# Kernel tuning notes

Hardware: AMD Instinct MI355X
Metric: run time of the kernel (lower is better)

## Reference

```python
import jax, jax.numpy as jnp
import numpy as np

B, T, E, H = 16, 1024, 1024, 16
DH = E // H  # 64, divisible by 4
THETA = 10000.0


def setup_inputs() -> dict:
    key = jax.random.key(0)
    ks = jax.random.split(key, 10)
    inp = {
        "hidden_states": jax.random.normal(ks[0], (B, T, E), dtype=jnp.float32),
        "rope_pos": jax.random.randint(ks[1], (B, T, 2), 0, 32, dtype=jnp.int32),
    }
    s = 0.02
    inp["Wq"] = jax.random.normal(ks[2], (E, E), dtype=jnp.float32) * s
    inp["bq"] = jnp.zeros((E,), dtype=jnp.float32)
    inp["Wk"] = jax.random.normal(ks[3], (E, E), dtype=jnp.float32) * s
    inp["bk"] = jnp.zeros((E,), dtype=jnp.float32)
    inp["Wv"] = jax.random.normal(ks[4], (E, E), dtype=jnp.float32) * s
    inp["bv"] = jnp.zeros((E,), dtype=jnp.float32)
    inp["Wo"] = jax.random.normal(ks[5], (E, E), dtype=jnp.float32) * s
    inp["bo"] = jnp.zeros((E,), dtype=jnp.float32)
    return inp


def _rotate_half(x):
    # interleaved pairs: (x0,x1,x2,x3,...) -> (-x1,x0,-x3,x2,...)
    x_even = x[..., ::2]
    x_odd = x[..., 1::2]
    return jnp.stack((-x_odd, x_even), axis=-1).reshape(x.shape)


def _apply_rope_2d(q, k, rope_pos, theta):
    Dh = q.shape[-1]
    half, quarter = Dh // 2, Dh // 4
    dtype = q.dtype
    idx = jnp.arange(quarter, dtype=dtype)
    inv = (theta ** (-2.0 * idx / quarter)).astype(dtype)  # [quarter]
    pos_h = rope_pos[..., 0].astype(dtype)[..., None]  # [B,T,1]
    pos_w = rope_pos[..., 1].astype(dtype)[..., None]
    ang_h = pos_h * inv  # [B,T,quarter]
    ang_w = pos_w * inv
    ri = lambda a: jnp.repeat(a, 2, axis=-1)[:, None]  # -> [B,1,T,half]
    cos_h, sin_h = ri(jnp.cos(ang_h)), ri(jnp.sin(ang_h))
    cos_w, sin_w = ri(jnp.cos(ang_w)), ri(jnp.sin(ang_w))
    q_h, q_w = q[..., :half], q[..., half:]
    k_h, k_w = k[..., :half], k[..., half:]
    q_h = q_h * cos_h + _rotate_half(q_h) * sin_h
    k_h = k_h * cos_h + _rotate_half(k_h) * sin_h
    q_w = q_w * cos_w + _rotate_half(q_w) * sin_w
    k_w = k_w * cos_w + _rotate_half(k_w) * sin_w
    return jnp.concatenate([q_h, q_w], axis=-1), jnp.concatenate([k_h, k_w], axis=-1)


def reference(hidden_states, rope_pos, Wq, bq, Wk, bk, Wv, bv, Wo, bo):
    b, t, e = hidden_states.shape
    scale = DH ** -0.5
    # torch nn.Linear: y = x @ W.T + b, W is [out, in]
    proj = lambda x, W, bias: jnp.einsum('bte,oe->bto', x, W) + bias
    q = proj(hidden_states, Wq, bq).reshape(b, t, H, DH).transpose(0, 2, 1, 3)
    k = proj(hidden_states, Wk, bk).reshape(b, t, H, DH).transpose(0, 2, 1, 3)
    v = proj(hidden_states, Wv, bv).reshape(b, t, H, DH).transpose(0, 2, 1, 3)
    q, k = _apply_rope_2d(q, k, rope_pos, THETA)
    # eager attention: scores in input dtype, softmax in float32
    scores = jnp.einsum('bhqd,bhkd->bhqk', q, k) * scale
    w = jax.nn.softmax(scores.astype(jnp.float32), axis=-1).astype(q.dtype)
    out = jnp.einsum('bhqk,bhkd->bhqd', w, v)
    out = out.transpose(0, 2, 1, 3).reshape(b, t, e)
    return jnp.einsum('bte,oe->bto', out, Wo) + bo
```

## Files before the change

kernel.cpp:

```cpp
#include <hip/hip_runtime.h>
#include <hip/hip_bf16.h>

#define B_  16
#define T_  1024
#define E_  1024
#define H_  16
#define DH_ 64

typedef short s16x8 __attribute__((ext_vector_type(8)));
typedef float f32x4 __attribute__((ext_vector_type(4)));
typedef unsigned short u16x4 __attribute__((ext_vector_type(4)));

__device__ __forceinline__ void async_cp16(const void* g, void* l) {
  __builtin_amdgcn_global_load_lds(
      (__attribute__((address_space(1))) unsigned int*)(g),
      (__attribute__((address_space(3))) unsigned int*)(l), 16, 0, 0);
}

__device__ __forceinline__ s16x8 frag8(const void* p) { return *(const s16x8*)p; }

__device__ __forceinline__ float fexp2(float x) {
#if __has_builtin(__builtin_amdgcn_exp2f)
  return __builtin_amdgcn_exp2f(x);
#else
  return exp2f(x);
#endif
}

__device__ __forceinline__ unsigned short f2bu(float x) {
  __hip_bfloat16 h = __float2bfloat16(x);
  return *reinterpret_cast<unsigned short*>(&h);
}

__device__ __forceinline__ float bu2f(unsigned short u) {
  __hip_bfloat16 h = *reinterpret_cast<__hip_bfloat16*>(&u);
  return __bfloat162float(h);
}

__global__ __launch_bounds__(256) void cast_all(const float* __restrict__ X,
                                                const float* __restrict__ Wq,
                                                const float* __restrict__ Wk,
                                                const float* __restrict__ Wv,
                                                const float* __restrict__ Wo,
                                                __hip_bfloat16* __restrict__ Xb,
                                                __hip_bfloat16* __restrict__ Wqkvb,
                                                __hip_bfloat16* __restrict__ Wob) {
  const int bid = blockIdx.x;
  const float* src;
  __hip_bfloat16* dst;
  int i;
  if (bid < 16384) {
    src = X; dst = Xb; i = bid * 256 + threadIdx.x;
  } else {
    const int wb = bid - 16384;
    const int w = wb >> 10;
    src = (w == 0) ? Wq : (w == 1) ? Wk : (w == 2) ? Wv : Wo;
    dst = (w == 3) ? Wob : Wqkvb + (size_t)w * 1048576;
    i = (wb & 1023) * 256 + threadIdx.x;
  }
  float4 v = ((const float4*)src)[i];
  u16x4 pk = {f2bu(v.x), f2bu(v.y), f2bu(v.z), f2bu(v.w)};
  *(u16x4*)(dst + (size_t)i * 4) = pk;
}

#define G8_ISSUE(SRC_, LOFF_, H_, D_, KT_)                                      \
  {                                                                             \
    _Pragma("unroll") for (int u_ = 0; u_ < 2; ++u_) {                          \
      const int ch_ = u_ * 8 + wave;                                            \
      async_cp16(SRC_ + (size_t)((H_)*128 + ch_ * 8) * 2048 + (KT_)*128,        \
                 smem + (D_)*65536 + (LOFF_) + (H_)*16384 + ch_ * 1024);        \
    }                                                                           \
  }

#define G8_READ_A(D_, S_)                                                       \
  {                                                                             \
    _Pragma("unroll") for (int i_ = 0; i_ < 4; ++i_) {                          \
      const char* rp_ = smem + (D_)*65536 + wrow * 16384 +                      \
                        ((S_)*64 + i_ * 16 + col) * 128;                        \
      af[i_][0] = frag8(rp_ + sw0);                                             \
      af[i_][1] = frag8(rp_ + sw1);                                             \
    }                                                                           \
  }

#define G8_READ_B(D_, T8_, BF_)                                                 \
  {                                                                             \
    _Pragma("unroll") for (int j_ = 0; j_ < 2; ++j_) {                          \
      const char* rp_ = smem + (D_)*65536 + 32768 + (wcol >> 1) * 16384 +       \
                        ((wcol & 1) * 64 + (T8_)*32 + j_ * 16 + col) * 128;     \
      BF_[j_][0] = frag8(rp_ + sw0);                                            \
      BF_[j_][1] = frag8(rp_ + sw1);                                            \
    }                                                                           \
  }

#define G8_MFMA(S_, T8_, BF_)                                                   \
  {                                                                             \
    __builtin_amdgcn_s_setprio(1);                                              \
    _Pragma("unroll") for (int i_ = 0; i_ < 4; ++i_)                            \
      _Pragma("unroll") for (int j_ = 0; j_ < 2; ++j_) {                        \
        acc[(S_)*4 + i_][(T8_)*2 + j_] = __builtin_amdgcn_mfma_f32_16x16x32_bf16( \
            af[i_][0], BF_[j_][0], acc[(S_)*4 + i_][(T8_)*2 + j_], 0, 0, 0);    \
        acc[(S_)*4 + i_][(T8_)*2 + j_] = __builtin_amdgcn_mfma_f32_16x16x32_bf16( \
            af[i_][1], BF_[j_][1], acc[(S_)*4 + i_][(T8_)*2 + j_], 0, 0, 0);    \
      }                                                                         \
    __builtin_amdgcn_s_setprio(0);                                              \
  }

#define G8_KTILE(D_, GA_, GB_, KTA_, KTB_, VM_)                                 \
  G8_READ_A(D_, 0)                                                              \
  G8_READ_B(D_, 0, bf0)                                                         \
  if (GA_) G8_ISSUE(Asrc, 0, 0, (D_) ^ 1, KTA_)                                 \
  __builtin_amdgcn_s_barrier();                                                 \
  G8_MFMA(0, 0, bf0)                                                            \
  __builtin_amdgcn_s_barrier();                                                 \
  G8_READ_B(D_, 1, bf1)                                                         \
  if (GA_) G8_ISSUE(Asrc, 0, 1, (D_) ^ 1, KTA_)                                 \
  __builtin_amdgcn_s_barrier();                                                 \
  G8_MFMA(0, 1, bf1)                                                            \
  __builtin_amdgcn_s_barrier();                                                 \
  G8_READ_A(D_, 1)                                                              \
  if (GB_) G8_ISSUE(Bsrc, 32768, 0, (D_), KTB_)                                 \
  __builtin_amdgcn_s_barrier();                                                 \
  G8_MFMA(1, 1, bf1)                                                            \
  __builtin_amdgcn_s_barrier();                                                 \
  if (GB_) G8_ISSUE(Bsrc, 32768, 1, (D_), KTB_)                                 \
  __builtin_amdgcn_s_barrier();                                                 \
  G8_MFMA(1, 0, bf0)                                                            \
  if (VM_) { asm volatile("s_waitcnt vmcnt(4)" ::: "memory"); }                 \
  else     { asm volatile("s_waitcnt vmcnt(0)" ::: "memory"); }                 \
  __builtin_amdgcn_s_barrier();

#define G8_CORE(APTR_, BPTR_)                                                   \
  __shared__ __align__(16) char smem[131072];                                   \
  const int tid = threadIdx.x;                                                  \
  const int lane = tid & 63, wave = tid >> 6;                                   \
  const int col = lane & 15, quad = lane >> 4;                                  \
  const int wrow = wave >> 2, wcol = wave & 3;                                  \
  const int r8 = lane >> 3;                                                     \
  const int gsw = (lane & 7) ^ r8;                                              \
  const int sw0 = (quad ^ (col & 7)) * 16;                                      \
  const int sw1 = ((quad + 4) ^ (col & 7)) * 16;                                \
  const char* Asrc = (const char*)(APTR_) + (size_t)(bm + r8) * 2048 + gsw * 16;\
  const char* Bsrc = (const char*)(BPTR_) + (size_t)(bn + r8) * 2048 + gsw * 16;\
  const f32x4 fzero = {0.f, 0.f, 0.f, 0.f};                                     \
  f32x4 acc[8][4];                                                              \
  _Pragma("unroll") for (int i_ = 0; i_ < 8; i_++)                              \
    _Pragma("unroll") for (int j_ = 0; j_ < 4; j_++) acc[i_][j_] = fzero;       \
  s16x8 af[4][2], bf0[2][2], bf1[2][2];                                         \
  G8_ISSUE(Bsrc, 32768, 0, 0, 0)                                                \
  G8_ISSUE(Bsrc, 32768, 1, 0, 0)                                                \
  G8_ISSUE(Asrc, 0, 0, 0, 0)                                                    \
  G8_ISSUE(Asrc, 0, 1, 0, 0)                                                    \
  G8_ISSUE(Bsrc, 32768, 0, 1, 1)                                                \
  G8_ISSUE(Bsrc, 32768, 1, 1, 1)                                                \
  asm volatile("s_waitcnt vmcnt(4)" ::: "memory");                              \
  __builtin_amdgcn_s_barrier();                                                 \
  _Pragma("clang loop unroll(disable)") for (int it = 0; it < 8; ++it) {        \
    const bool g7 = (it < 7);                                                   \
    G8_KTILE(0, true, g7, 2 * it + 1, 2 * it + 2, g7)                           \
    G8_KTILE(1, g7, g7, 2 * it + 2, 2 * it + 3, g7)                             \
  }

__global__ __launch_bounds__(512, 2) void gemm_qkv(const __hip_bfloat16* __restrict__ A,
                                                   const __hip_bfloat16* __restrict__ Wqkv,
                                                   const float* __restrict__ bq,
                                                   const float* __restrict__ bk,
                                                   const float* __restrict__ bv,
                                                   const int* __restrict__ pos,
                                                   __hip_bfloat16* __restrict__ Qb,
                                                   __hip_bfloat16* __restrict__ Kb,
                                                   __hip_bfloat16* __restrict__ Vt) {
  const int wg = (blockIdx.x & 7) * 96 + (blockIdx.x >> 3);
  const int bm = (wg & 63) << 8;
  const int bn = (wg >> 6) << 8;
  G8_CORE(A, Wqkv)

  const int seg = bn >> 10;
  const float* bp = (seg == 0) ? bq : (seg == 1) ? bk : bv;
  const int nbase = (bn & 1023) + wcol * 64;
  float bcol[4];
#pragma unroll
  for (int j = 0; j < 4; j++) bcol[j] = bp[nbase + j * 16 + col];
  if (seg < 2) {
    __syncthreads();
    float2* tab = (float2*)smem;
    {
      const int p_ = tid >> 4, f_ = tid & 15;
      const float inv = __expf((float)f_ * -1.1512925464970229f);
      float s_, c_;
      __sincosf((float)p_ * inv, &s_, &c_);
      tab[tid] = make_float2(c_, s_);
    }
    __syncthreads();
    const float SCL = (seg == 0) ? 0.18033688011112043f : 1.0f;
    __hip_bfloat16* P = (seg == 0) ? Qb : Kb;
    const int codd = col & 1;
#pragma unroll
    for (int mi = 0; mi < 8; mi++) {
      const int gr0 = bm + wrow * 128 + mi * 16 + quad * 4;
#pragma unroll
      for (int r = 0; r < 4; r++) {
        const int grow = gr0 + r;
        const int iph = pos[grow * 2 + 0];
        const int ipw = pos[grow * 2 + 1];
#pragma unroll
        for (int ni = 0; ni < 4; ni++) {
          const int f = ((ni & 1) << 3) + (col >> 1);
          const int p_ = (ni >= 2) ? ipw : iph;
          const float2 cs = tab[p_ * 16 + f];
          const float v = acc[mi][ni][r] + bcol[ni];
          const float vp = __shfl_xor(v, 1, 64);
          const float rot = codd ? (v * cs.x + vp * cs.y) : (v * cs.x - vp * cs.y);
          P[(size_t)grow * 1024 + nbase + ni * 16 + col] = __float2bfloat16(rot * SCL);
        }
      }
    }
  } else {
#pragma unroll
    for (int mi = 0; mi < 8; mi++) {
      const int gr0 = bm + wrow * 128 + mi * 16 + quad * 4;
      const int bb = gr0 >> 10, tt = gr0 & 1023;
#pragma unroll
      for (int ni = 0; ni < 4; ni++) {
        const int nc = nbase + ni * 16 + col;
        const int hh = nc >> 6, dd = nc & 63;
        u16x4 pk = {f2bu(acc[mi][ni][0] + bcol[ni]), f2bu(acc[mi][ni][1] + bcol[ni]),
                    f2bu(acc[mi][ni][2] + bcol[ni]), f2bu(acc[mi][ni][3] + bcol[ni])};
        *(u16x4*)(Vt + (((size_t)bb * H_ + hh) * DH_ + dd) * T_ + tt) = pk;
      }
    }
  }
}

__global__ __launch_bounds__(512, 2) void gemm_out(const __hip_bfloat16* __restrict__ A,
                                                   const __hip_bfloat16* __restrict__ Bw,
                                                   const float* __restrict__ bias,
                                                   float* __restrict__ Cout) {
  const int wg = (blockIdx.x & 7) * 32 + (blockIdx.x >> 3);
  const int bm = (wg & 63) << 8;
  const int bn = (wg >> 6) << 8;
  G8_CORE(A, Bw)

  const int nbase = bn + wcol * 64;
  float bcol[4];
#pragma unroll
  for (int j = 0; j < 4; j++) bcol[j] = bias[nbase + j * 16 + col];
#pragma unroll
  for (int mi = 0; mi < 8; mi++) {
    const int gr0 = bm + wrow * 128 + mi * 16 + quad * 4;
#pragma unroll
    for (int ni = 0; ni < 4; ni++) {
      const int gcol = nbase + ni * 16 + col;
#pragma unroll
      for (int r = 0; r < 4; r++)
        Cout[(size_t)(gr0 + r) * 1024 + gcol] = acc[mi][ni][r] + bcol[ni];
    }
  }
}

__global__ __launch_bounds__(256, 3) void attn_flash(const __hip_bfloat16* __restrict__ Q,
                                                     const __hip_bfloat16* __restrict__ Kt,
                                                     const __hip_bfloat16* __restrict__ Vt,
                                                     __hip_bfloat16* __restrict__ Oa) {
  __shared__ __align__(16) __hip_bfloat16 QP[128 * 72];
  __shared__ __align__(16) __hip_bfloat16 Ks[64 * 72];
  __shared__ __align__(16) __hip_bfloat16 Vs[64 * 72];

  const int bid = blockIdx.x;
  const int xcd = bid & 7, slot = bid >> 3;
  const int bh = xcd * 32 + (slot >> 3);
  const int qt = slot & 7;
  const int b = bh >> 4, h = bh & 15;
  const int tid = threadIdx.x;
  const int lane = tid & 63, wave = tid >> 6;
  const int col = lane & 15, quad = lane >> 4;

  const size_t qrow0 = (size_t)b * T_ + qt * 128;

#pragma unroll
  for (int cc = 0; cc < 4; ++cc) {
    int c = tid + cc * 256;
    int r = c >> 3, k8 = c & 7;
    const float4* src = (const float4*)((const char*)(Q + (qrow0 + r) * E_ + h * DH_)) + k8;
    *(float4*)((char*)QP + r * 144 + k8 * 16) = *src;
  }

  const char* Ksrc = (const char*)(Kt + (size_t)b * T_ * E_ + h * DH_);
  const char* Vsrc = (const char*)(Vt + ((size_t)b * H_ + h) * DH_ * (size_t)T_);
  const int sr = tid >> 3, sk8 = tid & 7;
  float4 kv[4];
#define LOADKV(KB_)                                                                  \
  {                                                                                  \
    kv[0] = *(const float4*)(Ksrc + (size_t)((KB_) + sr) * 2048 + sk8 * 16);         \
    kv[1] = *(const float4*)(Ksrc + (size_t)((KB_) + 32 + sr) * 2048 + sk8 * 16);    \
    kv[2] = *(const float4*)(Vsrc + (size_t)sr * 2048 + (KB_)*2 + sk8 * 16);         \
    kv[3] = *(const float4*)(Vsrc + (size_t)(32 + sr) * 2048 + (KB_)*2 + sk8 * 16);  \
  }
#define WRITEKV()                                                                    \
  {                                                                                  \
    *(float4*)((char*)Ks + sr * 144 + sk8 * 16) = kv[0];                             \
    *(float4*)((char*)Ks + (32 + sr) * 144 + sk8 * 16) = kv[1];                      \
    *(float4*)((char*)Vs + sr * 144 + sk8 * 16) = kv[2];                             \
    *(float4*)((char*)Vs + (32 + sr) * 144 + sk8 * 16) = kv[3];                      \
  }

  const f32x4 fzero = {0.f, 0.f, 0.f, 0.f};
  f32x4 o[2][4];
  float lr[2] = {0.f, 0.f};
#pragma unroll
  for (int g = 0; g < 2; g++)
#pragma unroll
    for (int j = 0; j < 4; j++) o[g][j] = fzero;
  s16x8 qf[2][2];
  char* Pw = (char*)QP + wave * 32 * 144;

  LOADKV(0)
  for (int kt2 = 0; kt2 < 16; ++kt2) {
    __syncthreads();
    WRITEKV()
    __syncthreads();
    if (kt2 == 0) {
#pragma unroll
      for (int g = 0; g < 2; g++) {
        qf[g][0] = frag8((const char*)QP + (g * 64 + wave * 16 + col) * 144 + quad * 16);
        qf[g][1] = frag8((const char*)QP + (g * 64 + wave * 16 + col) * 144 + 64 + quad * 16);
      }
      __syncthreads();
    }
    if (kt2 < 15) LOADKV((kt2 + 1) * 64)
    s16x8 kf[4][2];
#pragma unroll
    for (int ktile = 0; ktile < 4; ktile++) {
      kf[ktile][0] = frag8((const char*)Ks + (ktile * 16 + col) * 144 + quad * 16);
      kf[ktile][1] = frag8((const char*)Ks + (ktile * 16 + col) * 144 + 64 + quad * 16);
    }
#pragma unroll
    for (int g = 0; g < 2; g++) {
#pragma unroll
      for (int ktile = 0; ktile < 4; ktile++) {
        f32x4 d = fzero;
        d = __builtin_amdgcn_mfma_f32_16x16x32_bf16(kf[ktile][0], qf[g][0], d, 0, 0, 0);
        d = __builtin_amdgcn_mfma_f32_16x16x32_bf16(kf[ktile][1], qf[g][1], d, 0, 0, 0);
        float p0 = fexp2(d[0]), p1 = fexp2(d[1]), p2 = fexp2(d[2]), p3 = fexp2(d[3]);
        lr[g] += (p0 + p1) + (p2 + p3);
        u16x4 pk = {f2bu(p0), f2bu(p1), f2bu(p2), f2bu(p3)};
        *(u16x4*)(Pw + (g * 16 + col) * 144 + ktile * 32 + quad * 8) = pk;
      }
    }
    s16x8 vf[4][2];
#pragma unroll
    for (int jm = 0; jm < 4; jm++) {
      vf[jm][0] = frag8((const char*)Vs + (jm * 16 + col) * 144 + quad * 16);
      vf[jm][1] = frag8((const char*)Vs + (jm * 16 + col) * 144 + 64 + quad * 16);
    }
#pragma unroll
    for (int g = 0; g < 2; g++) {
      s16x8 pf0 = frag8(Pw + (g * 16 + col) * 144 + quad * 16);
      s16x8 pf1 = frag8(Pw + (g * 16 + col) * 144 + 64 + quad * 16);
#pragma unroll
      for (int jm = 0; jm < 4; jm++) {
        o[g][jm] = __builtin_amdgcn_mfma_f32_16x16x32_bf16(vf[jm][0], pf0, o[g][jm], 0, 0, 0);
        o[g][jm] = __builtin_amdgcn_mfma_f32_16x16x32_bf16(vf[jm][1], pf1, o[g][jm], 0, 0, 0);
      }
    }
  }
#undef LOADKV
#undef WRITEKV
#pragma unroll
  for (int g = 0; g < 2; g++) {
    lr[g] += __shfl_xor(lr[g], 16, 64);
    lr[g] += __shfl_xor(lr[g], 32, 64);
  }
#pragma unroll
  for (int g = 0; g < 2; g++) {
    float invl = 1.f / lr[g];
    size_t grow = qrow0 + g * 64 + wave * 16 + col;
    char* obase = (char*)(Oa + grow * E_ + h * DH_);
#pragma unroll
    for (int jm = 0; jm < 4; jm++) {
      u16x4 pk = {f2bu(o[g][jm][0] * invl), f2bu(o[g][jm][1] * invl),
                  f2bu(o[g][jm][2] * invl), f2bu(o[g][jm][3] * invl)};
      *(u16x4*)(obase + jm * 32 + quad * 8) = pk;
    }
  }
}

extern "C" void kernel_launch(void* const* d_in, const int* in_sizes, int n_in,
                              void* d_out, int out_size, void* d_ws, size_t ws_size,
                              hipStream_t stream) {
  const float* X   = (const float*)d_in[0];
  const int*   pos = (const int*)d_in[1];
  const float* Wq  = (const float*)d_in[2];
  const float* bq  = (const float*)d_in[3];
  const float* Wk  = (const float*)d_in[4];
  const float* bk  = (const float*)d_in[5];
  const float* Wv  = (const float*)d_in[6];
  const float* bv  = (const float*)d_in[7];
  const float* Wo  = (const float*)d_in[8];
  const float* bo  = (const float*)d_in[9];
  float* out = (float*)d_out;

  char* ws = (char*)d_ws;
  const size_t MB = 1024 * 1024;
  __hip_bfloat16* Xb    = (__hip_bfloat16*)(ws + 0 * MB);
  __hip_bfloat16* Qb    = (__hip_bfloat16*)(ws + 32 * MB);
  __hip_bfloat16* Kb    = (__hip_bfloat16*)(ws + 64 * MB);
  __hip_bfloat16* Vtb   = (__hip_bfloat16*)(ws + 96 * MB);
  __hip_bfloat16* Wqkvb = (__hip_bfloat16*)(ws + 128 * MB);
  __hip_bfloat16* Wob   = (__hip_bfloat16*)(ws + 136 * MB);
  __hip_bfloat16* Ab    = Xb;

  cast_all<<<20480, 256, 0, stream>>>(X, Wq, Wk, Wv, Wo, Xb, Wqkvb, Wob);

  gemm_qkv<<<768, 512, 0, stream>>>(Xb, Wqkvb, bq, bk, bv, pos, Qb, Kb, Vtb);

  attn_flash<<<2048, 256, 0, stream>>>(Qb, Kb, Vtb, Ab);

  gemm_out<<<256, 512, 0, stream>>>(Ab, Wob, bo, out);
}
```

Measured before the change: 433.8 us.

## Double-buffer K/V tiles via async global-to-LDS loads with XOR swizzle

Replaces the register-staged K/V loads (global to register, then register to LDS) in the flash attention kernel with direct async global_load_lds copies into a double-buffered LDS area. The next tile is fetched while the current one is computed, so each iteration needs one barrier instead of two. Padded rows are replaced by an XOR-swizzled 128-byte row layout to avoid LDS bank conflicts. LDS use per block grows, which could strain the 3-blocks-per-CU occupancy target. Correctness depends on the barrier also waiting for the outstanding async copies.

```diff
diff --git a/kernel.cpp b/kernel.cpp
--- a/kernel.cpp
+++ b/kernel.cpp
@@ -30,11 +30,6 @@
 __device__ __forceinline__ unsigned short f2bu(float x) {
   __hip_bfloat16 h = __float2bfloat16(x);
   return *reinterpret_cast<unsigned short*>(&h);
-}
-
-__device__ __forceinline__ float bu2f(unsigned short u) {
-  __hip_bfloat16 h = *reinterpret_cast<__hip_bfloat16*>(&u);
-  return __bfloat162float(h);
 }
 
 __global__ __launch_bounds__(256) void cast_all(const float* __restrict__ X,
@@ -262,8 +257,7 @@
                                                      const __hip_bfloat16* __restrict__ Vt,
                                                      __hip_bfloat16* __restrict__ Oa) {
   __shared__ __align__(16) __hip_bfloat16 QP[128 * 72];
-  __shared__ __align__(16) __hip_bfloat16 Ks[64 * 72];
-  __shared__ __align__(16) __hip_bfloat16 Vs[64 * 72];
+  __shared__ __align__(16) char KV[2][2][8192];
 
   const int bid = blockIdx.x;
   const int xcd = bid & 7, slot = bid >> 3;
@@ -273,9 +267,27 @@
   const int tid = threadIdx.x;
   const int lane = tid & 63, wave = tid >> 6;
   const int col = lane & 15, quad = lane >> 4;
+  const int r8 = lane >> 3;
+  const int gsw = ((lane & 7) ^ r8) * 16;
+  const int sw0 = (quad ^ (col & 7)) * 16;
+  const int sw1 = ((quad + 4) ^ (col & 7)) * 16;
 
   const size_t qrow0 = (size_t)b * T_ + qt * 128;
 
+  const char* Kbase = (const char*)(Kt + (size_t)b * T_ * E_ + h * DH_);
+  const char* Vbase = (const char*)(Vt + ((size_t)b * H_ + h) * DH_ * (size_t)T_);
+#define STAGE_KV(KB_, D_)                                                          \
+  {                                                                                \
+    _Pragma("unroll") for (int u_ = 0; u_ < 2; ++u_) {                             \
+      const int ch_ = u_ * 4 + wave;                                               \
+      async_cp16(Kbase + (size_t)((KB_) + ch_ * 8 + r8) * 2048 + gsw,              \
+                 &KV[D_][0][ch_ * 1024]);                                          \
+      async_cp16(Vbase + (size_t)(ch_ * 8 + r8) * 2048 + (KB_)*2 + gsw,            \
+                 &KV[D_][1][ch_ * 1024]);                                          \
+    }                                                                              \
+  }
+
+  STAGE_KV(0, 0)
 #pragma unroll
   for (int cc = 0; cc < 4; ++cc) {
     int c = tid + cc * 256;
@@ -283,25 +295,15 @@
     const float4* src = (const float4*)((const char*)(Q + (qrow0 + r) * E_ + h * DH_)) + k8;
     *(float4*)((char*)QP + r * 144 + k8 * 16) = *src;
   }
-
-  const char* Ksrc = (const char*)(Kt + (size_t)b * T_ * E_ + h * DH_);
-  const char* Vsrc = (const char*)(Vt + ((size_t)b * H_ + h) * DH_ * (size_t)T_);
-  const int sr = tid >> 3, sk8 = tid & 7;
-  float4 kv[4];
-#define LOADKV(KB_)                                                                  \
-  {                                                                                  \
-    kv[0] = *(const float4*)(Ksrc + (size_t)((KB_) + sr) * 2048 + sk8 * 16);         \
-    kv[1] = *(const float4*)(Ksrc + (size_t)((KB_) + 32 + sr) * 2048 + sk8 * 16);    \
-    kv[2] = *(const float4*)(Vsrc + (size_t)sr * 2048 + (KB_)*2 + sk8 * 16);         \
-    kv[3] = *(const float4*)(Vsrc + (size_t)(32 + sr) * 2048 + (KB_)*2 + sk8 * 16);  \
-  }
-#define WRITEKV()                                                                    \
-  {                                                                                  \
-    *(float4*)((char*)Ks + sr * 144 + sk8 * 16) = kv[0];                             \
-    *(float4*)((char*)Ks + (32 + sr) * 144 + sk8 * 16) = kv[1];                      \
-    *(float4*)((char*)Vs + sr * 144 + sk8 * 16) = kv[2];                             \
-    *(float4*)((char*)Vs + (32 + sr) * 144 + sk8 * 16) = kv[3];                      \
-  }
+  __syncthreads();
+
+  s16x8 qf[2][2];
+#pragma unroll
+  for (int g = 0; g < 2; g++) {
+    qf[g][0] = frag8((const char*)QP + (g * 64 + wave * 16 + col) * 144 + quad * 16);
+    qf[g][1] = frag8((const char*)QP + (g * 64 + wave * 16 + col) * 144 + 64 + quad * 16);
+  }
+  __syncthreads();
 
   const f32x4 fzero = {0.f, 0.f, 0.f, 0.f};
   f32x4 o[2][4];
@@ -310,37 +312,26 @@
   for (int g = 0; g < 2; g++)
 #pragma unroll
     for (int j = 0; j < 4; j++) o[g][j] = fzero;
-  s16x8 qf[2][2];
   char* Pw = (char*)QP + wave * 32 * 144;
 
-  LOADKV(0)
   for (int kt2 = 0; kt2 < 16; ++kt2) {
-    __syncthreads();
-    WRITEKV()
-    __syncthreads();
-    if (kt2 == 0) {
-#pragma unroll
-      for (int g = 0; g < 2; g++) {
-        qf[g][0] = frag8((const char*)QP + (g * 64 + wave * 16 + col) * 144 + quad * 16);
-        qf[g][1] = frag8((const char*)QP + (g * 64 + wave * 16 + col) * 144 + 64 + quad * 16);
-      }
-      __syncthreads();
-    }
-    if (kt2 < 15) LOADKV((kt2 + 1) * 64)
+    const int d = kt2 & 1;
+    if (kt2 < 15) STAGE_KV((kt2 + 1) * 64, d ^ 1)
     s16x8 kf[4][2];
 #pragma unroll
     for (int ktile = 0; ktile < 4; ktile++) {
-      kf[ktile][0] = frag8((const char*)Ks + (ktile * 16 + col) * 144 + quad * 16);
-      kf[ktile][1] = frag8((const char*)Ks + (ktile * 16 + col) * 144 + 64 + quad * 16);
+      const char* kp = &KV[d][0][(ktile * 16 + col) * 128];
+      kf[ktile][0] = frag8(kp + sw0);
+      kf[ktile][1] = frag8(kp + sw1);
     }
 #pragma unroll
     for (int g = 0; g < 2; g++) {
 #pragma unroll
       for (int ktile = 0; ktile < 4; ktile++) {
-        f32x4 d = fzero;
-        d = __builtin_amdgcn_mfma_f32_16x16x32_bf16(kf[ktile][0], qf[g][0], d, 0, 0, 0);
-        d = __builtin_amdgcn_mfma_f32_16x16x32_bf16(kf[ktile][1], qf[g][1], d, 0, 0, 0);
-        float p0 = fexp2(d[0]), p1 = fexp2(d[1]), p2 = fexp2(d[2]), p3 = fexp2(d[3]);
+        f32x4 dacc = fzero;
+        dacc = __builtin_amdgcn_mfma_f32_16x16x32_bf16(kf[ktile][0], qf[g][0], dacc, 0, 0, 0);
+        dacc = __builtin_amdgcn_mfma_f32_16x16x32_bf16(kf[ktile][1], qf[g][1], dacc, 0, 0, 0);
+        float p0 = fexp2(dacc[0]), p1 = fexp2(dacc[1]), p2 = fexp2(dacc[2]), p3 = fexp2(dacc[3]);
         lr[g] += (p0 + p1) + (p2 + p3);
         u16x4 pk = {f2bu(p0), f2bu(p1), f2bu(p2), f2bu(p3)};
         *(u16x4*)(Pw + (g * 16 + col) * 144 + ktile * 32 + quad * 8) = pk;
@@ -349,8 +340,9 @@
     s16x8 vf[4][2];
 #pragma unroll
     for (int jm = 0; jm < 4; jm++) {
-      vf[jm][0] = frag8((const char*)Vs + (jm * 16 + col) * 144 + quad * 16);
-      vf[jm][1] = frag8((const char*)Vs + (jm * 16 + col) * 144 + 64 + quad * 16);
+      const char* vp = &KV[d][1][(jm * 16 + col) * 128];
+      vf[jm][0] = frag8(vp + sw0);
+      vf[jm][1] = frag8(vp + sw1);
     }
 #pragma unroll
     for (int g = 0; g < 2; g++) {
@@ -362,9 +354,9 @@
         o[g][jm] = __builtin_amdgcn_mfma_f32_16x16x32_bf16(vf[jm][1], pf1, o[g][jm], 0, 0, 0);
       }
     }
-  }
-#undef LOADKV
-#undef WRITEKV
+    __syncthreads();
+  }
+#undef STAGE_KV
 #pragma unroll
   for (int g = 0; g < 2; g++) {
     lr[g] += __shfl_xor(lr[g], 16, 64);
```

After: 366.2 us. -15.6%, faster.
